# Kernel tuning notes

Hardware: AMD Instinct MI355X
Metric: run time of the kernel (lower is better)

Reference implementation:

```python
import jax, jax.numpy as jnp
import numpy as np

B, S, D = 2, 2048, 1024
H = 16
HD = D // H  # 64


def setup_inputs() -> dict:
    key = jax.random.key(0)
    ks = jax.random.split(key, 6)
    x = jax.random.normal(ks[0], (B, S, D), dtype=jnp.float32)
    sc = 1.0 / np.sqrt(D)
    Wq = jax.random.normal(ks[1], (D, D), dtype=jnp.float32) * sc
    Wk = jax.random.normal(ks[2], (D, D), dtype=jnp.float32) * sc
    Wv = jax.random.normal(ks[3], (D, D), dtype=jnp.float32) * sc
    Wo = jax.random.normal(ks[4], (D, D), dtype=jnp.float32) * sc
    bo = jax.random.normal(ks[5], (D,), dtype=jnp.float32) * 0.01
    return {"x": x, "Wq": Wq, "Wk": Wk, "Wv": Wv, "Wo": Wo, "bo": bo}


def reference(x, Wq, Wk, Wv, Wo, bo):
    b, s, d = x.shape
    # projections (torch Linear: y = x @ W.T; weights here stored as [d_in, d_out])
    Q = (x @ Wq).reshape(b, s, H, HD).transpose(0, 2, 1, 3)  # [b,h,s,hd]
    K = (x @ Wk).reshape(b, s, H, HD).transpose(0, 2, 1, 3)
    V = (x @ Wv).reshape(b, s, H, HD).transpose(0, 2, 1, 3)
    scores = jnp.einsum("bhqd,bhkd->bhqk", Q, K) / np.sqrt(HD)
    causal = jnp.triu(jnp.ones((s, s), dtype=bool), k=1)  # True above diagonal
    scores = jnp.where(causal[None, None], -jnp.inf, scores)
    attn = jax.nn.softmax(scores, axis=-1)
    # dropout_rate = 0.0 -> identity (eval-mode reference)
    ctx = jnp.einsum("bhqk,bhkd->bhqd", attn, V)
    ctx = ctx.transpose(0, 2, 1, 3).reshape(b, s, d)
    return ctx @ Wo + bo
```

## Files before the change

kernel.cpp:

```cpp
#include <hip/hip_runtime.h>
#include <hip/hip_bf16.h>

#define B_  2
#define S_  2048
#define D_  1024
#define H_  16
#define HD_ 64
#define M_  (B_*S_)

typedef __attribute__((ext_vector_type(8))) short short8;
typedef __attribute__((ext_vector_type(4))) float f32x4;

#define MFMA16(a, b, c) __builtin_amdgcn_mfma_f32_16x16x32_bf16((a), (b), (c), 0, 0, 0)

static __device__ inline short f2bf(float f) {
    union { float f; unsigned u; } v; v.f = f;
    unsigned r = v.u + 0x7FFFu + ((v.u >> 16) & 1u);
    return (short)(r >> 16);
}

static __device__ __forceinline__ float fexp2(float x) {
    float r;
    asm volatile("v_exp_f32 %0, %1\n\ts_nop 1" : "=v"(r) : "v"(x));
    return r;
}

static __device__ __forceinline__ unsigned cvt_pk_bf16(float lo, float hi) {
    unsigned r;
    asm volatile("v_cvt_pk_bf16_f32 %0, %1, %2" : "=v"(r) : "v"(lo), "v"(hi));
    return r;
}

static __device__ __forceinline__ void gl_lds16(const short* g, short* l) {
    __builtin_amdgcn_global_load_lds(
        (const __attribute__((address_space(1))) void*)g,
        (__attribute__((address_space(3))) void*)l, 16, 0, 0);
}

__global__ void prep_kernel(const float* __restrict__ x,
                            const float* __restrict__ Wq, const float* __restrict__ Wk,
                            const float* __restrict__ Wv, const float* __restrict__ Wo,
                            short* __restrict__ xb,
                            short* __restrict__ Wqkvt, short* __restrict__ Wot) {
    int z = blockIdx.z;
    if (z == 4) {
        int bid = blockIdx.y * 32 + blockIdx.x;
        int base = bid * 1024 + threadIdx.x;
#pragma unroll
        for (int it = 0; it < 4; ++it) {
            int i = base + it * 256;
            float4 v = ((const float4*)x)[i];
            short4 o;
            o.x = f2bf(v.x); o.y = f2bf(v.y); o.z = f2bf(v.z); o.w = f2bf(v.w);
            ((short4*)xb)[i] = o;
        }
        return;
    }
    __shared__ float tile[32][33];
    const float* W = (z == 0) ? Wq : (z == 1) ? Wk : (z == 2) ? Wv : Wo;
    short* Wt = (z == 3) ? Wot : (Wqkvt + ((size_t)z << 20));
    int tx = threadIdx.x & 31, ty = threadIdx.x >> 5;
    int n0 = blockIdx.x * 32, k0 = blockIdx.y * 32;
#pragma unroll
    for (int i = 0; i < 4; ++i)
        tile[ty + 8 * i][tx] = W[(size_t)(k0 + ty + 8 * i) * D_ + n0 + tx];
    __syncthreads();
#pragma unroll
    for (int i = 0; i < 4; ++i)
        Wt[(size_t)(n0 + ty + 8 * i) * D_ + k0 + tx] = f2bf(tile[tx][ty + 8 * i]);
}

__global__ __launch_bounds__(256) void gemm_qkv(const short* __restrict__ A,
                                                const short* __restrict__ Bt,
                                                short* __restrict__ out) {
    __shared__ __align__(16) short Asm[2][128 * 32];
    __shared__ __align__(16) short Bsm[2][128 * 32];
    const int NBX = 3;
    int X = blockIdx.x & 7, t = blockIdx.x >> 3;
    int bm = t / NBX, bn = X * NBX + t % NBX;
    int tid = threadIdx.x, l = tid & 63, w = tid >> 6;
    int lhi = l >> 4, llo = l & 15;
    int wm = w >> 1, wn = w & 1;

    f32x4 acc[4][4];
#pragma unroll
    for (int m = 0; m < 4; ++m)
#pragma unroll
        for (int n = 0; n < 4; ++n) acc[m][n] = (f32x4){0.f, 0.f, 0.f, 0.f};

    const short* Ag = A + (size_t)(bm * 128) * 1024;
    const short* Bg = Bt + (size_t)(bn * 128) * 1024;
    int c0 = tid, c1 = 256 + tid;
    int r0 = ((c0 >> 5) << 3) | (c0 & 7), s0 = ((c0 >> 3) & 3) ^ (r0 & 3);
    int r1 = ((c1 >> 5) << 3) | (c1 & 7), s1 = ((c1 >> 3) & 3) ^ (r1 & 3);

    auto stage = [&](int buf, int k0) {
        gl_lds16(Ag + (size_t)r0 * 1024 + k0 + s0 * 8, &Asm[buf][c0 * 8]);
        gl_lds16(Ag + (size_t)r1 * 1024 + k0 + s1 * 8, &Asm[buf][c1 * 8]);
        gl_lds16(Bg + (size_t)r0 * 1024 + k0 + s0 * 8, &Bsm[buf][c0 * 8]);
        gl_lds16(Bg + (size_t)r1 * 1024 + k0 + s1 * 8, &Bsm[buf][c1 * 8]);
    };

    int cia[4], cib[4];
#pragma unroll
    for (int m = 0; m < 4; ++m) {
        int row = wm * 64 + m * 16 + llo;
        cia[m] = ((row >> 3) << 5) | (((lhi ^ row) & 3) << 3) | (row & 7);
    }
#pragma unroll
    for (int n = 0; n < 4; ++n) {
        int row = wn * 64 + n * 16 + llo;
        cib[n] = ((row >> 3) << 5) | (((lhi ^ row) & 3) << 3) | (row & 7);
    }

    stage(0, 0);
    for (int i = 0; i < 32; ++i) {
        asm volatile("s_waitcnt vmcnt(0)" ::: "memory");
        __builtin_amdgcn_s_barrier();
        asm volatile("" ::: "memory");
        if (i + 1 < 32) stage((i + 1) & 1, (i + 1) * 32);
        int cur = i & 1;
        short8 af[4], bf[4];
#pragma unroll
        for (int m = 0; m < 4; ++m) af[m] = *(const short8*)&Asm[cur][cia[m] * 8];
#pragma unroll
        for (int n = 0; n < 4; ++n) bf[n] = *(const short8*)&Bsm[cur][cib[n] * 8];
#pragma unroll
        for (int m = 0; m < 4; ++m)
#pragma unroll
            for (int n = 0; n < 4; ++n)
                acc[m][n] = MFMA16(af[m], bf[n], acc[m][n]);
    }

    int rowb = bm * 128 + wm * 64, colb = bn * 128 + wn * 64;
#pragma unroll
    for (int m = 0; m < 4; ++m) {
#pragma unroll
        for (int n = 0; n < 4; ++n) {
            int col = colb + n * 16 + llo;
#pragma unroll
            for (int j = 0; j < 4; ++j) {
                int row = rowb + m * 16 + lhi * 4 + j;
                float v = acc[m][n][j];
                int proj = col >> 10, n1 = col & 1023;
                int h = n1 >> 6, hd = n1 & 63;
                int b = row >> 11, s = row & 2047;
                size_t off;
                if (proj == 0)
                    off = ((size_t)(b * 16 + h) * 2048 + s) * 64 + hd;
                else if (proj == 1)
                    off = (size_t)M_ * D_ + ((size_t)(b * 16 + h) * 2048 + s) * 64 + hd;
                else
                    off = (size_t)2 * M_ * D_ + ((size_t)(b * 16 + h) * 64 + hd) * 2048 + s;
                out[off] = f2bf(v);
            }
        }
    }
}

__global__ __launch_bounds__(256, 6) void gemm_out(const short* __restrict__ A,
                                                   const short* __restrict__ Bt,
                                                   const float* __restrict__ bias,
                                                   float* __restrict__ out) {
    __shared__ __align__(16) short Asm[2][64 * 32];
    __shared__ __align__(16) short Bsm[2][128 * 32];
    int bn = blockIdx.x & 7, bm = blockIdx.x >> 3;
    int tid = threadIdx.x, l = tid & 63, w = tid >> 6;
    int lhi = l >> 4, llo = l & 15;

    f32x4 acc[4][2];
#pragma unroll
    for (int m = 0; m < 4; ++m)
#pragma unroll
        for (int n = 0; n < 2; ++n) acc[m][n] = (f32x4){0.f, 0.f, 0.f, 0.f};

    const short* Ag = A + (size_t)(bm * 64) * 1024;
    const short* Bg = Bt + (size_t)(bn * 128) * 1024;
    int ca = tid;
    int ra = ((ca >> 5) << 3) | (ca & 7), sa = ((ca >> 3) & 3) ^ (ra & 3);
    int cb0 = tid, cb1 = tid + 256;
    int rb0 = ((cb0 >> 5) << 3) | (cb0 & 7), sb0 = ((cb0 >> 3) & 3) ^ (rb0 & 3);
    int rb1 = ((cb1 >> 5) << 3) | (cb1 & 7), sb1 = ((cb1 >> 3) & 3) ^ (rb1 & 3);

    auto stage = [&](int buf, int k0) {
        gl_lds16(Ag + (size_t)ra * 1024 + k0 + sa * 8, &Asm[buf][ca * 8]);
        gl_lds16(Bg + (size_t)rb0 * 1024 + k0 + sb0 * 8, &Bsm[buf][cb0 * 8]);
        gl_lds16(Bg + (size_t)rb1 * 1024 + k0 + sb1 * 8, &Bsm[buf][cb1 * 8]);
    };

    int cia[4], cib[2];
#pragma unroll
    for (int m = 0; m < 4; ++m) {
        int row = m * 16 + llo;
        cia[m] = ((row >> 3) << 5) | (((lhi ^ row) & 3) << 3) | (row & 7);
    }
#pragma unroll
    for (int n = 0; n < 2; ++n) {
        int row = w * 32 + n * 16 + llo;
        cib[n] = ((row >> 3) << 5) | (((lhi ^ row) & 3) << 3) | (row & 7);
    }

    stage(0, 0);
    for (int i = 0; i < 32; ++i) {
        asm volatile("s_waitcnt vmcnt(0)" ::: "memory");
        __builtin_amdgcn_s_barrier();
        asm volatile("" ::: "memory");
        if (i + 1 < 32) stage((i + 1) & 1, (i + 1) * 32);
        int cur = i & 1;
        short8 af[4], bf[2];
#pragma unroll
        for (int m = 0; m < 4; ++m) af[m] = *(const short8*)&Asm[cur][cia[m] * 8];
#pragma unroll
        for (int n = 0; n < 2; ++n) bf[n] = *(const short8*)&Bsm[cur][cib[n] * 8];
#pragma unroll
        for (int m = 0; m < 4; ++m)
#pragma unroll
            for (int n = 0; n < 2; ++n)
                acc[m][n] = MFMA16(af[m], bf[n], acc[m][n]);
    }

    int rowb = bm * 64, colb = bn * 128 + w * 32;
#pragma unroll
    for (int m = 0; m < 4; ++m)
#pragma unroll
        for (int n = 0; n < 2; ++n) {
            int col = colb + n * 16 + llo;
#pragma unroll
            for (int j = 0; j < 4; ++j) {
                int row = rowb + m * 16 + lhi * 4 + j;
                out[(size_t)row * 1024 + col] = acc[m][n][j] + bias[col];
            }
        }
}

__global__ __launch_bounds__(512) void attn_kernel(const short* __restrict__ Q,
                                                   const short* __restrict__ Kg,
                                                   const short* __restrict__ Vt,
                                                   short* __restrict__ ctx) {
    __shared__ __align__(16) char kvbuf[2][16384];
    __shared__ __align__(16) char plds[8][2048];
    int tid = threadIdx.x, w = tid >> 6, l = tid & 63;
    int lhi = l >> 4, llo = l & 15;
    int bh = blockIdx.x & 31, qp = blockIdx.x >> 5;
    int b = bh >> 4, h = bh & 15;
    char* pb = plds[w];

    const short* Qh = Q + (size_t)bh * S_ * HD_;
    const short* Kh = Kg + (size_t)bh * S_ * HD_;
    const short* Vh = Vt + (size_t)bh * HD_ * S_;

    int qbA = qp, qbB = 15 - qp;
    int NTA = 2 * qp + 2;
    const int NT = 34;

    int srow = tid >> 3;
    int ssrc = (16 * (tid & 7)) ^ ((srow & 7) << 4);
    auto stage = [&](char* buf, int c0) {
        gl_lds16(Kh + (size_t)(c0 + srow) * HD_ + (ssrc >> 1), (short*)(buf + tid * 16));
        gl_lds16(Vh + (size_t)srow * S_ + c0 + (ssrc >> 1), (short*)(buf + 8192 + tid * 16));
    };

    f32x4 O[4];
#pragma unroll
    for (int n = 0; n < 4; ++n) O[n] = (f32x4){0.f, 0.f, 0.f, 0.f};
    float lpart[4] = {0.f, 0.f, 0.f, 0.f};

    auto writeOut = [&](int qb) {
        int qbs = qb * 128 + w * 16;
#pragma unroll
        for (int j = 0; j < 4; ++j) {
            float ls = lpart[j];
            ls += __shfl_xor(ls, 1);
            ls += __shfl_xor(ls, 2);
            ls += __shfl_xor(ls, 4);
            ls += __shfl_xor(ls, 8);
            float inv = 1.0f / ls;
            int row = qbs + lhi * 4 + j;
            size_t base = ((size_t)(b * S_ + row)) * D_ + h * HD_;
#pragma unroll
            for (int n = 0; n < 4; ++n)
                ctx[base + n * 16 + llo] = f2bf(O[n][j] * inv);
        }
    };

    const float SC = 0.18033688f;
    const float M2 = 17.312340f;

    int qbase = qbA * 128 + w * 16;
    short8 aq0 = *(const short8*)(Qh + (size_t)(qbase + llo) * HD_ + 8 * lhi);
    short8 aq1 = *(const short8*)(Qh + (size_t)(qbase + llo) * HD_ + 32 + 8 * lhi);

    stage(kvbuf[0], 0);

    for (int i = 0; i < NT; ++i) {
        asm volatile("s_waitcnt vmcnt(0)" ::: "memory");
        __builtin_amdgcn_s_barrier();
        asm volatile("" ::: "memory");
        int kt = (i < NTA) ? i : i - NTA;
        int c0 = kt * 64;
        if (i + 1 < NT) {
            int ni = i + 1;
            int nkt = (ni < NTA) ? ni : ni - NTA;
            stage(kvbuf[ni & 1], nkt * 64);
        }
        const char* kb = kvbuf[i & 1];
        const char* vb = kb + 8192;

        if (c0 <= qbase + 15) {
            f32x4 sc4[4];
#pragma unroll
            for (int cb = 0; cb < 4; ++cb) {
                int row = cb * 16 + llo;
                int sw = (row & 7) << 4;
                short8 kf0 = *(const short8*)(kb + row * 128 + ((16 * lhi) ^ sw));
                short8 kf1 = *(const short8*)(kb + row * 128 + ((64 + 16 * lhi) ^ sw));
                f32x4 z = (f32x4){0.f, 0.f, 0.f, 0.f};
                z = MFMA16(aq0, kf0, z);
                z = MFMA16(aq1, kf1, z);
                sc4[cb] = z;
            }
            bool diag = (c0 + 63 > qbase);
#pragma unroll
            for (int j = 0; j < 4; ++j) {
                int qr = qbase + lhi * 4 + j;
                float v0 = fmaf(sc4[0][j], SC, -M2);
                float v1 = fmaf(sc4[1][j], SC, -M2);
                float v2 = fmaf(sc4[2][j], SC, -M2);
                float v3 = fmaf(sc4[3][j], SC, -M2);
                if (diag) {
                    if (c0 + llo > qr)      v0 = -1e30f;
                    if (c0 + 16 + llo > qr) v1 = -1e30f;
                    if (c0 + 32 + llo > qr) v2 = -1e30f;
                    if (c0 + 48 + llo > qr) v3 = -1e30f;
                }
                float p0 = fexp2(v0), p1 = fexp2(v1);
                float p2 = fexp2(v2), p3 = fexp2(v3);
                lpart[j] += (p0 + p1) + (p2 + p3);
                unsigned pk01 = cvt_pk_bf16(p0, p1);
                unsigned pk23 = cvt_pk_bf16(p2, p3);
                int r = lhi * 4 + j;
                char* rb = pb + r * 128;
                int sw = (r & 7) << 4;
                *(short*)(rb + ((2 * llo) ^ sw))      = (short)(pk01);
                *(short*)(rb + ((2 * llo + 32) ^ sw)) = (short)(pk01 >> 16);
                *(short*)(rb + ((2 * llo + 64) ^ sw)) = (short)(pk23);
                *(short*)(rb + ((2 * llo + 96) ^ sw)) = (short)(pk23 >> 16);
            }
            int swr = (llo & 7) << 4;
            short8 pa0 = *(const short8*)(pb + llo * 128 + ((16 * lhi) ^ swr));
            short8 pa1 = *(const short8*)(pb + llo * 128 + ((64 + 16 * lhi) ^ swr));
#pragma unroll
            for (int n = 0; n < 4; ++n) {
                int row = n * 16 + llo;
                int sw = (row & 7) << 4;
                short8 vf0 = *(const short8*)(vb + row * 128 + ((16 * lhi) ^ sw));
                short8 vf1 = *(const short8*)(vb + row * 128 + ((64 + 16 * lhi) ^ sw));
                O[n] = MFMA16(pa0, vf0, O[n]);
                O[n] = MFMA16(pa1, vf1, O[n]);
            }
        }

        if (i == NTA - 1) {
            writeOut(qbA);
#pragma unroll
            for (int n = 0; n < 4; ++n) O[n] = (f32x4){0.f, 0.f, 0.f, 0.f};
            lpart[0] = lpart[1] = lpart[2] = lpart[3] = 0.f;
            qbase = qbB * 128 + w * 16;
            aq0 = *(const short8*)(Qh + (size_t)(qbase + llo) * HD_ + 8 * lhi);
            aq1 = *(const short8*)(Qh + (size_t)(qbase + llo) * HD_ + 32 + 8 * lhi);
        }
    }
    writeOut(qbB);
}

extern "C" void kernel_launch(void* const* d_in, const int* in_sizes, int n_in,
                              void* d_out, int out_size, void* d_ws, size_t ws_size,
                              hipStream_t stream) {
    const float* x  = (const float*)d_in[0];
    const float* Wq = (const float*)d_in[1];
    const float* Wk = (const float*)d_in[2];
    const float* Wv = (const float*)d_in[3];
    const float* Wo = (const float*)d_in[4];
    const float* bo = (const float*)d_in[5];
    float* out = (float*)d_out;

    char* ws = (char*)d_ws;
    short* xb    = (short*)(ws);
    short* Wqkvt = (short*)(ws + (size_t)(8 << 20));
    short* Wot   = (short*)(ws + (size_t)(14 << 20));
    short* Qb    = (short*)(ws + (size_t)(16 << 20));
    short* Kb    = Qb + (size_t)M_ * D_;
    short* Vtb   = Qb + (size_t)2 * M_ * D_;
    short* ctx   = xb;

    prep_kernel<<<dim3(32, 32, 5), 256, 0, stream>>>(x, Wq, Wk, Wv, Wo, xb, Wqkvt, Wot);
    gemm_qkv<<<768, 256, 0, stream>>>(xb, Wqkvt, Qb);
    attn_kernel<<<256, 512, 0, stream>>>(Qb, Kb, Vtb, ctx);
    gemm_out<<<512, 256, 0, stream>>>(ctx, Wot, bo, out);
}
```

Measured before the change: 133.8 us.

## Give each attention wave two query sub-tiles and permute V layout for vector P stores

```diff
diff --git a/kernel.cpp b/kernel.cpp
--- a/kernel.cpp
+++ b/kernel.cpp
@@ -150,8 +150,10 @@
                     off = ((size_t)(b * 16 + h) * 2048 + s) * 64 + hd;
                 else if (proj == 1)
                     off = (size_t)M_ * D_ + ((size_t)(b * 16 + h) * 2048 + s) * 64 + hd;
-                else
-                    off = (size_t)2 * M_ * D_ + ((size_t)(b * 16 + h) * 64 + hd) * 2048 + s;
+                else {
+                    int sp = (s & ~63) | (4 * (s & 15) + ((s >> 4) & 3));
+                    off = (size_t)2 * M_ * D_ + ((size_t)(b * 16 + h) * 64 + hd) * 2048 + sp;
+                }
                 out[off] = f2bf(v);
             }
         }
@@ -233,12 +235,12 @@
         }
 }
 
-__global__ __launch_bounds__(512) void attn_kernel(const short* __restrict__ Q,
+__global__ __launch_bounds__(256) void attn_kernel(const short* __restrict__ Q,
                                                    const short* __restrict__ Kg,
                                                    const short* __restrict__ Vt,
                                                    short* __restrict__ ctx) {
     __shared__ __align__(16) char kvbuf[2][16384];
-    __shared__ __align__(16) char plds[8][2048];
+    __shared__ __align__(16) char plds[4][4096];
     int tid = threadIdx.x, w = tid >> 6, l = tid & 63;
     int lhi = l >> 4, llo = l & 15;
     int bh = blockIdx.x & 31, qp = blockIdx.x >> 5;
@@ -253,42 +255,55 @@
     int NTA = 2 * qp + 2;
     const int NT = 34;
 
-    int srow = tid >> 3;
-    int ssrc = (16 * (tid & 7)) ^ ((srow & 7) << 4);
+    int cc0 = tid, cc1 = tid + 256;
+    int r0 = cc0 >> 3, s0 = (16 * (cc0 & 7)) ^ ((r0 & 7) << 4);
+    int r1 = cc1 >> 3, s1 = (16 * (cc1 & 7)) ^ ((r1 & 7) << 4);
     auto stage = [&](char* buf, int c0) {
-        gl_lds16(Kh + (size_t)(c0 + srow) * HD_ + (ssrc >> 1), (short*)(buf + tid * 16));
-        gl_lds16(Vh + (size_t)srow * S_ + c0 + (ssrc >> 1), (short*)(buf + 8192 + tid * 16));
+        gl_lds16(Kh + (size_t)(c0 + r0) * HD_ + (s0 >> 1), (short*)(buf + cc0 * 16));
+        gl_lds16(Kh + (size_t)(c0 + r1) * HD_ + (s1 >> 1), (short*)(buf + cc1 * 16));
+        gl_lds16(Vh + (size_t)r0 * S_ + c0 + (s0 >> 1), (short*)(buf + 8192 + cc0 * 16));
+        gl_lds16(Vh + (size_t)r1 * S_ + c0 + (s1 >> 1), (short*)(buf + 8192 + cc1 * 16));
     };
 
-    f32x4 O[4];
-#pragma unroll
-    for (int n = 0; n < 4; ++n) O[n] = (f32x4){0.f, 0.f, 0.f, 0.f};
-    float lpart[4] = {0.f, 0.f, 0.f, 0.f};
-
-    auto writeOut = [&](int qb) {
-        int qbs = qb * 128 + w * 16;
-#pragma unroll
-        for (int j = 0; j < 4; ++j) {
-            float ls = lpart[j];
-            ls += __shfl_xor(ls, 1);
-            ls += __shfl_xor(ls, 2);
-            ls += __shfl_xor(ls, 4);
-            ls += __shfl_xor(ls, 8);
-            float inv = 1.0f / ls;
-            int row = qbs + lhi * 4 + j;
-            size_t base = ((size_t)(b * S_ + row)) * D_ + h * HD_;
-#pragma unroll
-            for (int n = 0; n < 4; ++n)
-                ctx[base + n * 16 + llo] = f2bf(O[n][j] * inv);
-        }
-    };
+    f32x4 O[2][4];
+    float lpart[2][4];
+#pragma unroll
+    for (int g = 0; g < 2; ++g)
+#pragma unroll
+        for (int n = 0; n < 4; ++n) {
+            O[g][n] = (f32x4){0.f, 0.f, 0.f, 0.f};
+            lpart[g][n] = 0.f;
+        }
 
     const float SC = 0.18033688f;
     const float M2 = 17.312340f;
 
-    int qbase = qbA * 128 + w * 16;
-    short8 aq0 = *(const short8*)(Qh + (size_t)(qbase + llo) * HD_ + 8 * lhi);
-    short8 aq1 = *(const short8*)(Qh + (size_t)(qbase + llo) * HD_ + 32 + 8 * lhi);
+    int qbw = qbA * 128 + w * 32;
+    short8 aq[2][2];
+#pragma unroll
+    for (int g = 0; g < 2; ++g) {
+        aq[g][0] = *(const short8*)(Qh + (size_t)(qbw + g * 16 + llo) * HD_ + 8 * lhi);
+        aq[g][1] = *(const short8*)(Qh + (size_t)(qbw + g * 16 + llo) * HD_ + 32 + 8 * lhi);
+    }
+
+    auto writeOut = [&](int qb) {
+#pragma unroll
+        for (int g = 0; g < 2; ++g)
+#pragma unroll
+            for (int j = 0; j < 4; ++j) {
+                float ls = lpart[g][j];
+                ls += __shfl_xor(ls, 1);
+                ls += __shfl_xor(ls, 2);
+                ls += __shfl_xor(ls, 4);
+                ls += __shfl_xor(ls, 8);
+                float inv = 1.0f / ls;
+                int row = qb * 128 + w * 32 + g * 16 + lhi * 4 + j;
+                size_t base = ((size_t)(b * S_ + row)) * D_ + h * HD_;
+#pragma unroll
+                for (int n = 0; n < 4; ++n)
+                    ctx[base + n * 16 + llo] = f2bf(O[g][n][j] * inv);
+            }
+    };
 
     stage(kvbuf[0], 0);
 
@@ -306,68 +321,91 @@
         const char* kb = kvbuf[i & 1];
         const char* vb = kb + 8192;
 
-        if (c0 <= qbase + 15) {
-            f32x4 sc4[4];
+        if (c0 <= qbw + 31) {
+            bool act0 = (c0 <= qbw + 15);
+            f32x4 sc4[2][4];
 #pragma unroll
             for (int cb = 0; cb < 4; ++cb) {
                 int row = cb * 16 + llo;
                 int sw = (row & 7) << 4;
                 short8 kf0 = *(const short8*)(kb + row * 128 + ((16 * lhi) ^ sw));
                 short8 kf1 = *(const short8*)(kb + row * 128 + ((64 + 16 * lhi) ^ sw));
-                f32x4 z = (f32x4){0.f, 0.f, 0.f, 0.f};
-                z = MFMA16(aq0, kf0, z);
-                z = MFMA16(aq1, kf1, z);
-                sc4[cb] = z;
-            }
-            bool diag = (c0 + 63 > qbase);
-#pragma unroll
-            for (int j = 0; j < 4; ++j) {
-                int qr = qbase + lhi * 4 + j;
-                float v0 = fmaf(sc4[0][j], SC, -M2);
-                float v1 = fmaf(sc4[1][j], SC, -M2);
-                float v2 = fmaf(sc4[2][j], SC, -M2);
-                float v3 = fmaf(sc4[3][j], SC, -M2);
-                if (diag) {
-                    if (c0 + llo > qr)      v0 = -1e30f;
-                    if (c0 + 16 + llo > qr) v1 = -1e30f;
-                    if (c0 + 32 + llo > qr) v2 = -1e30f;
-                    if (c0 + 48 + llo > qr) v3 = -1e30f;
+                f32x4 z1 = (f32x4){0.f, 0.f, 0.f, 0.f};
+                z1 = MFMA16(aq[1][0], kf0, z1);
+                z1 = MFMA16(aq[1][1], kf1, z1);
+                sc4[1][cb] = z1;
+                if (act0) {
+                    f32x4 z0 = (f32x4){0.f, 0.f, 0.f, 0.f};
+                    z0 = MFMA16(aq[0][0], kf0, z0);
+                    z0 = MFMA16(aq[0][1], kf1, z0);
+                    sc4[0][cb] = z0;
                 }
-                float p0 = fexp2(v0), p1 = fexp2(v1);
-                float p2 = fexp2(v2), p3 = fexp2(v3);
-                lpart[j] += (p0 + p1) + (p2 + p3);
-                unsigned pk01 = cvt_pk_bf16(p0, p1);
-                unsigned pk23 = cvt_pk_bf16(p2, p3);
-                int r = lhi * 4 + j;
-                char* rb = pb + r * 128;
-                int sw = (r & 7) << 4;
-                *(short*)(rb + ((2 * llo) ^ sw))      = (short)(pk01);
-                *(short*)(rb + ((2 * llo + 32) ^ sw)) = (short)(pk01 >> 16);
-                *(short*)(rb + ((2 * llo + 64) ^ sw)) = (short)(pk23);
-                *(short*)(rb + ((2 * llo + 96) ^ sw)) = (short)(pk23 >> 16);
-            }
-            int swr = (llo & 7) << 4;
-            short8 pa0 = *(const short8*)(pb + llo * 128 + ((16 * lhi) ^ swr));
-            short8 pa1 = *(const short8*)(pb + llo * 128 + ((64 + 16 * lhi) ^ swr));
+            }
+#pragma unroll
+            for (int g = 0; g < 2; ++g) {
+                if (g == 0 && !act0) continue;
+                bool diag = (c0 + 63 > qbw + g * 16);
+#pragma unroll
+                for (int j = 0; j < 4; ++j) {
+                    int qr = qbw + g * 16 + lhi * 4 + j;
+                    float v0 = fmaf(sc4[g][0][j], SC, -M2);
+                    float v1 = fmaf(sc4[g][1][j], SC, -M2);
+                    float v2 = fmaf(sc4[g][2][j], SC, -M2);
+                    float v3 = fmaf(sc4[g][3][j], SC, -M2);
+                    if (diag) {
+                        if (c0 + llo > qr)      v0 = -1e30f;
+                        if (c0 + 16 + llo > qr) v1 = -1e30f;
+                        if (c0 + 32 + llo > qr) v2 = -1e30f;
+                        if (c0 + 48 + llo > qr) v3 = -1e30f;
+                    }
+                    float p0 = fexp2(v0), p1 = fexp2(v1);
+                    float p2 = fexp2(v2), p3 = fexp2(v3);
+                    lpart[g][j] += (p0 + p1) + (p2 + p3);
+                    uint2 pk;
+                    pk.x = cvt_pk_bf16(p0, p1);
+                    pk.y = cvt_pk_bf16(p2, p3);
+                    int r = g * 16 + lhi * 4 + j;
+                    *(uint2*)(pb + r * 128 + ((8 * llo) ^ ((r & 7) << 4))) = pk;
+                }
+            }
+            short8 pa[2][2];
+#pragma unroll
+            for (int g = 0; g < 2; ++g) {
+                int rp = g * 16 + llo;
+                int swp = (rp & 7) << 4;
+                pa[g][0] = *(const short8*)(pb + rp * 128 + ((16 * lhi) ^ swp));
+                pa[g][1] = *(const short8*)(pb + rp * 128 + ((64 + 16 * lhi) ^ swp));
+            }
 #pragma unroll
             for (int n = 0; n < 4; ++n) {
                 int row = n * 16 + llo;
                 int sw = (row & 7) << 4;
                 short8 vf0 = *(const short8*)(vb + row * 128 + ((16 * lhi) ^ sw));
                 short8 vf1 = *(const short8*)(vb + row * 128 + ((64 + 16 * lhi) ^ sw));
-                O[n] = MFMA16(pa0, vf0, O[n]);
-                O[n] = MFMA16(pa1, vf1, O[n]);
+                O[1][n] = MFMA16(pa[1][0], vf0, O[1][n]);
+                O[1][n] = MFMA16(pa[1][1], vf1, O[1][n]);
+                if (act0) {
+                    O[0][n] = MFMA16(pa[0][0], vf0, O[0][n]);
+                    O[0][n] = MFMA16(pa[0][1], vf1, O[0][n]);
+                }
             }
         }
 
         if (i == NTA - 1) {
             writeOut(qbA);
 #pragma unroll
-            for (int n = 0; n < 4; ++n) O[n] = (f32x4){0.f, 0.f, 0.f, 0.f};
-            lpart[0] = lpart[1] = lpart[2] = lpart[3] = 0.f;
-            qbase = qbB * 128 + w * 16;
-            aq0 = *(const short8*)(Qh + (size_t)(qbase + llo) * HD_ + 8 * lhi);
-            aq1 = *(const short8*)(Qh + (size_t)(qbase + llo) * HD_ + 32 + 8 * lhi);
+            for (int g = 0; g < 2; ++g)
+#pragma unroll
+                for (int n = 0; n < 4; ++n) {
+                    O[g][n] = (f32x4){0.f, 0.f, 0.f, 0.f};
+                    lpart[g][n] = 0.f;
+                }
+            qbw = qbB * 128 + w * 32;
+#pragma unroll
+            for (int g = 0; g < 2; ++g) {
+                aq[g][0] = *(const short8*)(Qh + (size_t)(qbw + g * 16 + llo) * HD_ + 8 * lhi);
+                aq[g][1] = *(const short8*)(Qh + (size_t)(qbw + g * 16 + llo) * HD_ + 32 + 8 * lhi);
+            }
         }
     }
     writeOut(qbB);
@@ -395,6 +433,6 @@
 
     prep_kernel<<<dim3(32, 32, 5), 256, 0, stream>>>(x, Wq, Wk, Wv, Wo, xb, Wqkvt, Wot);
     gemm_qkv<<<768, 256, 0, stream>>>(xb, Wqkvt, Qb);
-    attn_kernel<<<256, 512, 0, stream>>>(Qb, Kb, Vtb, ctx);
+    attn_kernel<<<256, 256, 0, stream>>>(Qb, Kb, Vtb, ctx);
     gemm_out<<<512, 256, 0, stream>>>(ctx, Wot, bo, out);
 }
```

Result: slower. 175.7 us (+31.3%).

## Split attention into 64-row query blocks with 4 waves, vectorize P LDS writes

Applied to the files above, without the earlier changes.

```diff
diff --git a/kernel.cpp b/kernel.cpp
--- a/kernel.cpp
+++ b/kernel.cpp
@@ -150,8 +150,10 @@
                     off = ((size_t)(b * 16 + h) * 2048 + s) * 64 + hd;
                 else if (proj == 1)
                     off = (size_t)M_ * D_ + ((size_t)(b * 16 + h) * 2048 + s) * 64 + hd;
-                else
-                    off = (size_t)2 * M_ * D_ + ((size_t)(b * 16 + h) * 64 + hd) * 2048 + s;
+                else {
+                    int sp = (s & ~63) | (4 * (s & 15) + ((s >> 4) & 3));
+                    off = (size_t)2 * M_ * D_ + ((size_t)(b * 16 + h) * 64 + hd) * 2048 + sp;
+                }
                 out[off] = f2bf(v);
             }
         }
@@ -233,15 +235,15 @@
         }
 }
 
-__global__ __launch_bounds__(512) void attn_kernel(const short* __restrict__ Q,
-                                                   const short* __restrict__ Kg,
-                                                   const short* __restrict__ Vt,
-                                                   short* __restrict__ ctx) {
+__global__ __launch_bounds__(256, 4) void attn_kernel(const short* __restrict__ Q,
+                                                      const short* __restrict__ Kg,
+                                                      const short* __restrict__ Vt,
+                                                      short* __restrict__ ctx) {
     __shared__ __align__(16) char kvbuf[2][16384];
-    __shared__ __align__(16) char plds[8][2048];
+    __shared__ __align__(16) char plds[4][2048];
     int tid = threadIdx.x, w = tid >> 6, l = tid & 63;
     int lhi = l >> 4, llo = l & 15;
-    int bh = blockIdx.x & 31, qp = blockIdx.x >> 5;
+    int bh = blockIdx.x & 31, p = blockIdx.x >> 5;
     int b = bh >> 4, h = bh & 15;
     char* pb = plds[w];
 
@@ -249,15 +251,18 @@
     const short* Kh = Kg + (size_t)bh * S_ * HD_;
     const short* Vh = Vt + (size_t)bh * HD_ * S_;
 
-    int qbA = qp, qbB = 15 - qp;
-    int NTA = 2 * qp + 2;
-    const int NT = 34;
-
-    int srow = tid >> 3;
-    int ssrc = (16 * (tid & 7)) ^ ((srow & 7) << 4);
+    int qsA = p, qsB = 31 - p;
+    int NTA = p + 1;
+    const int NT = 33;
+
+    int cc0 = tid, cc1 = tid + 256;
+    int r0 = cc0 >> 3, s0 = (16 * (cc0 & 7)) ^ ((r0 & 7) << 4);
+    int r1 = cc1 >> 3, s1 = (16 * (cc1 & 7)) ^ ((r1 & 7) << 4);
     auto stage = [&](char* buf, int c0) {
-        gl_lds16(Kh + (size_t)(c0 + srow) * HD_ + (ssrc >> 1), (short*)(buf + tid * 16));
-        gl_lds16(Vh + (size_t)srow * S_ + c0 + (ssrc >> 1), (short*)(buf + 8192 + tid * 16));
+        gl_lds16(Kh + (size_t)(c0 + r0) * HD_ + (s0 >> 1), (short*)(buf + cc0 * 16));
+        gl_lds16(Kh + (size_t)(c0 + r1) * HD_ + (s1 >> 1), (short*)(buf + cc1 * 16));
+        gl_lds16(Vh + (size_t)r0 * S_ + c0 + (s0 >> 1), (short*)(buf + 8192 + cc0 * 16));
+        gl_lds16(Vh + (size_t)r1 * S_ + c0 + (s1 >> 1), (short*)(buf + 8192 + cc1 * 16));
     };
 
     f32x4 O[4];
@@ -265,8 +270,7 @@
     for (int n = 0; n < 4; ++n) O[n] = (f32x4){0.f, 0.f, 0.f, 0.f};
     float lpart[4] = {0.f, 0.f, 0.f, 0.f};
 
-    auto writeOut = [&](int qb) {
-        int qbs = qb * 128 + w * 16;
+    auto writeOut = [&](int qbase) {
 #pragma unroll
         for (int j = 0; j < 4; ++j) {
             float ls = lpart[j];
@@ -275,7 +279,7 @@
             ls += __shfl_xor(ls, 4);
             ls += __shfl_xor(ls, 8);
             float inv = 1.0f / ls;
-            int row = qbs + lhi * 4 + j;
+            int row = qbase + lhi * 4 + j;
             size_t base = ((size_t)(b * S_ + row)) * D_ + h * HD_;
 #pragma unroll
             for (int n = 0; n < 4; ++n)
@@ -286,7 +290,7 @@
     const float SC = 0.18033688f;
     const float M2 = 17.312340f;
 
-    int qbase = qbA * 128 + w * 16;
+    int qbase = qsA * 64 + w * 16;
     short8 aq0 = *(const short8*)(Qh + (size_t)(qbase + llo) * HD_ + 8 * lhi);
     short8 aq1 = *(const short8*)(Qh + (size_t)(qbase + llo) * HD_ + 32 + 8 * lhi);
 
@@ -336,15 +340,11 @@
                 float p0 = fexp2(v0), p1 = fexp2(v1);
                 float p2 = fexp2(v2), p3 = fexp2(v3);
                 lpart[j] += (p0 + p1) + (p2 + p3);
-                unsigned pk01 = cvt_pk_bf16(p0, p1);
-                unsigned pk23 = cvt_pk_bf16(p2, p3);
+                uint2 pk;
+                pk.x = cvt_pk_bf16(p0, p1);
+                pk.y = cvt_pk_bf16(p2, p3);
                 int r = lhi * 4 + j;
-                char* rb = pb + r * 128;
-                int sw = (r & 7) << 4;
-                *(short*)(rb + ((2 * llo) ^ sw))      = (short)(pk01);
-                *(short*)(rb + ((2 * llo + 32) ^ sw)) = (short)(pk01 >> 16);
-                *(short*)(rb + ((2 * llo + 64) ^ sw)) = (short)(pk23);
-                *(short*)(rb + ((2 * llo + 96) ^ sw)) = (short)(pk23 >> 16);
+                *(uint2*)(pb + r * 128 + ((8 * llo) ^ ((r & 7) << 4))) = pk;
             }
             int swr = (llo & 7) << 4;
             short8 pa0 = *(const short8*)(pb + llo * 128 + ((16 * lhi) ^ swr));
@@ -361,16 +361,16 @@
         }
 
         if (i == NTA - 1) {
-            writeOut(qbA);
+            writeOut(qsA * 64 + w * 16);
 #pragma unroll
             for (int n = 0; n < 4; ++n) O[n] = (f32x4){0.f, 0.f, 0.f, 0.f};
             lpart[0] = lpart[1] = lpart[2] = lpart[3] = 0.f;
-            qbase = qbB * 128 + w * 16;
+            qbase = qsB * 64 + w * 16;
             aq0 = *(const short8*)(Qh + (size_t)(qbase + llo) * HD_ + 8 * lhi);
             aq1 = *(const short8*)(Qh + (size_t)(qbase + llo) * HD_ + 32 + 8 * lhi);
         }
     }
-    writeOut(qbB);
+    writeOut(qsB * 64 + w * 16);
 }
 
 extern "C" void kernel_launch(void* const* d_in, const int* in_sizes, int n_in,
@@ -395,6 +395,6 @@
 
     prep_kernel<<<dim3(32, 32, 5), 256, 0, stream>>>(x, Wq, Wk, Wv, Wo, xb, Wqkvt, Wot);
     gemm_qkv<<<768, 256, 0, stream>>>(xb, Wqkvt, Qb);
-    attn_kernel<<<256, 512, 0, stream>>>(Qb, Kb, Vtb, ctx);
+    attn_kernel<<<512, 256, 0, stream>>>(Qb, Kb, Vtb, ctx);
     gemm_out<<<512, 256, 0, stream>>>(ctx, Wot, bo, out);
 }
```

After: 137.1 us. 1.02x slower.

## Load GEMM A operand directly from global into registers, staging only B in LDS

Applied to the files above, without the earlier changes.

```diff
diff --git a/kernel.cpp b/kernel.cpp
--- a/kernel.cpp
+++ b/kernel.cpp
@@ -73,11 +73,10 @@
 __global__ __launch_bounds__(256) void gemm_qkv(const short* __restrict__ A,
                                                 const short* __restrict__ Bt,
                                                 short* __restrict__ out) {
-    __shared__ __align__(16) short Asm[2][128 * 32];
     __shared__ __align__(16) short Bsm[2][128 * 32];
     const int NBX = 3;
-    int X = blockIdx.x & 7, t = blockIdx.x >> 3;
-    int bm = t / NBX, bn = X * NBX + t % NBX;
+    int X = blockIdx.x & 7, t0 = blockIdx.x >> 3;
+    int bm = t0 / NBX, bn = X * NBX + t0 % NBX;
     int tid = threadIdx.x, l = tid & 63, w = tid >> 6;
     int lhi = l >> 4, llo = l & 15;
     int wm = w >> 1, wn = w & 1;
@@ -90,46 +89,54 @@
 
     const short* Ag = A + (size_t)(bm * 128) * 1024;
     const short* Bg = Bt + (size_t)(bn * 128) * 1024;
+    const short* Ap = Ag + (size_t)(wm * 64 + llo) * 1024 + 8 * lhi;
     int c0 = tid, c1 = 256 + tid;
     int r0 = ((c0 >> 5) << 3) | (c0 & 7), s0 = ((c0 >> 3) & 3) ^ (r0 & 3);
     int r1 = ((c1 >> 5) << 3) | (c1 & 7), s1 = ((c1 >> 3) & 3) ^ (r1 & 3);
 
-    auto stage = [&](int buf, int k0) {
-        gl_lds16(Ag + (size_t)r0 * 1024 + k0 + s0 * 8, &Asm[buf][c0 * 8]);
-        gl_lds16(Ag + (size_t)r1 * 1024 + k0 + s1 * 8, &Asm[buf][c1 * 8]);
+    auto stageB = [&](int buf, int k0) {
         gl_lds16(Bg + (size_t)r0 * 1024 + k0 + s0 * 8, &Bsm[buf][c0 * 8]);
         gl_lds16(Bg + (size_t)r1 * 1024 + k0 + s1 * 8, &Bsm[buf][c1 * 8]);
     };
-
-    int cia[4], cib[4];
-#pragma unroll
-    for (int m = 0; m < 4; ++m) {
-        int row = wm * 64 + m * 16 + llo;
-        cia[m] = ((row >> 3) << 5) | (((lhi ^ row) & 3) << 3) | (row & 7);
-    }
+    auto loadA = [&](short8* dst, int k0) {
+#pragma unroll
+        for (int m = 0; m < 4; ++m)
+            dst[m] = *(const short8*)(Ap + (size_t)m * 16 * 1024 + k0);
+    };
+
+    int cib[4];
 #pragma unroll
     for (int n = 0; n < 4; ++n) {
         int row = wn * 64 + n * 16 + llo;
         cib[n] = ((row >> 3) << 5) | (((lhi ^ row) & 3) << 3) | (row & 7);
     }
 
-    stage(0, 0);
-    for (int i = 0; i < 32; ++i) {
+    auto compute = [&](const short8* af, const short* bs) {
+        short8 bf[4];
+#pragma unroll
+        for (int n = 0; n < 4; ++n) bf[n] = *(const short8*)&bs[cib[n] * 8];
+#pragma unroll
+        for (int m = 0; m < 4; ++m)
+#pragma unroll
+            for (int n = 0; n < 4; ++n)
+                acc[m][n] = MFMA16(af[m], bf[n], acc[m][n]);
+    };
+
+    short8 afA[4], afB[4];
+    stageB(0, 0);
+    loadA(afA, 0);
+#pragma unroll 1
+    for (int t = 0; t < 16; ++t) {
         asm volatile("s_waitcnt vmcnt(0)" ::: "memory");
         __builtin_amdgcn_s_barrier();
         asm volatile("" ::: "memory");
-        if (i + 1 < 32) stage((i + 1) & 1, (i + 1) * 32);
-        int cur = i & 1;
-        short8 af[4], bf[4];
-#pragma unroll
-        for (int m = 0; m < 4; ++m) af[m] = *(const short8*)&Asm[cur][cia[m] * 8];
-#pragma unroll
-        for (int n = 0; n < 4; ++n) bf[n] = *(const short8*)&Bsm[cur][cib[n] * 8];
-#pragma unroll
-        for (int m = 0; m < 4; ++m)
-#pragma unroll
-            for (int n = 0; n < 4; ++n)
-                acc[m][n] = MFMA16(af[m], bf[n], acc[m][n]);
+        if (2 * t + 1 < 32) { stageB(1, (2 * t + 1) * 32); loadA(afB, (2 * t + 1) * 32); }
+        compute(afA, Bsm[0]);
+        asm volatile("s_waitcnt vmcnt(0)" ::: "memory");
+        __builtin_amdgcn_s_barrier();
+        asm volatile("" ::: "memory");
+        if (2 * t + 2 < 32) { stageB(0, (2 * t + 2) * 32); loadA(afA, (2 * t + 2) * 32); }
+        compute(afB, Bsm[1]);
     }
 
     int rowb = bm * 128 + wm * 64, colb = bn * 128 + wn * 64;
@@ -158,11 +165,10 @@
     }
 }
 
-__global__ __launch_bounds__(256, 6) void gemm_out(const short* __restrict__ A,
+__global__ __launch_bounds__(256, 4) void gemm_out(const short* __restrict__ A,
                                                    const short* __restrict__ Bt,
                                                    const float* __restrict__ bias,
                                                    float* __restrict__ out) {
-    __shared__ __align__(16) short Asm[2][64 * 32];
     __shared__ __align__(16) short Bsm[2][128 * 32];
     int bn = blockIdx.x & 7, bm = blockIdx.x >> 3;
     int tid = threadIdx.x, l = tid & 63, w = tid >> 6;
@@ -176,47 +182,54 @@
 
     const short* Ag = A + (size_t)(bm * 64) * 1024;
     const short* Bg = Bt + (size_t)(bn * 128) * 1024;
-    int ca = tid;
-    int ra = ((ca >> 5) << 3) | (ca & 7), sa = ((ca >> 3) & 3) ^ (ra & 3);
-    int cb0 = tid, cb1 = tid + 256;
-    int rb0 = ((cb0 >> 5) << 3) | (cb0 & 7), sb0 = ((cb0 >> 3) & 3) ^ (rb0 & 3);
-    int rb1 = ((cb1 >> 5) << 3) | (cb1 & 7), sb1 = ((cb1 >> 3) & 3) ^ (rb1 & 3);
-
-    auto stage = [&](int buf, int k0) {
-        gl_lds16(Ag + (size_t)ra * 1024 + k0 + sa * 8, &Asm[buf][ca * 8]);
-        gl_lds16(Bg + (size_t)rb0 * 1024 + k0 + sb0 * 8, &Bsm[buf][cb0 * 8]);
-        gl_lds16(Bg + (size_t)rb1 * 1024 + k0 + sb1 * 8, &Bsm[buf][cb1 * 8]);
-    };
-
-    int cia[4], cib[2];
-#pragma unroll
-    for (int m = 0; m < 4; ++m) {
-        int row = m * 16 + llo;
-        cia[m] = ((row >> 3) << 5) | (((lhi ^ row) & 3) << 3) | (row & 7);
-    }
+    const short* Ap = Ag + (size_t)llo * 1024 + 8 * lhi;
+    int c0 = tid, c1 = 256 + tid;
+    int r0 = ((c0 >> 5) << 3) | (c0 & 7), s0 = ((c0 >> 3) & 3) ^ (r0 & 3);
+    int r1 = ((c1 >> 5) << 3) | (c1 & 7), s1 = ((c1 >> 3) & 3) ^ (r1 & 3);
+
+    auto stageB = [&](int buf, int k0) {
+        gl_lds16(Bg + (size_t)r0 * 1024 + k0 + s0 * 8, &Bsm[buf][c0 * 8]);
+        gl_lds16(Bg + (size_t)r1 * 1024 + k0 + s1 * 8, &Bsm[buf][c1 * 8]);
+    };
+    auto loadA = [&](short8* dst, int k0) {
+#pragma unroll
+        for (int m = 0; m < 4; ++m)
+            dst[m] = *(const short8*)(Ap + (size_t)m * 16 * 1024 + k0);
+    };
+
+    int cib[2];
 #pragma unroll
     for (int n = 0; n < 2; ++n) {
         int row = w * 32 + n * 16 + llo;
         cib[n] = ((row >> 3) << 5) | (((lhi ^ row) & 3) << 3) | (row & 7);
     }
 
-    stage(0, 0);
-    for (int i = 0; i < 32; ++i) {
+    auto compute = [&](const short8* af, const short* bs) {
+        short8 bf[2];
+#pragma unroll
+        for (int n = 0; n < 2; ++n) bf[n] = *(const short8*)&bs[cib[n] * 8];
+#pragma unroll
+        for (int m = 0; m < 4; ++m)
+#pragma unroll
+            for (int n = 0; n < 2; ++n)
+                acc[m][n] = MFMA16(af[m], bf[n], acc[m][n]);
+    };
+
+    short8 afA[4], afB[4];
+    stageB(0, 0);
+    loadA(afA, 0);
+#pragma unroll 1
+    for (int t = 0; t < 16; ++t) {
         asm volatile("s_waitcnt vmcnt(0)" ::: "memory");
         __builtin_amdgcn_s_barrier();
         asm volatile("" ::: "memory");
-        if (i + 1 < 32) stage((i + 1) & 1, (i + 1) * 32);
-        int cur = i & 1;
-        short8 af[4], bf[2];
-#pragma unroll
-        for (int m = 0; m < 4; ++m) af[m] = *(const short8*)&Asm[cur][cia[m] * 8];
-#pragma unroll
-        for (int n = 0; n < 2; ++n) bf[n] = *(const short8*)&Bsm[cur][cib[n] * 8];
-#pragma unroll
-        for (int m = 0; m < 4; ++m)
-#pragma unroll
-            for (int n = 0; n < 2; ++n)
-                acc[m][n] = MFMA16(af[m], bf[n], acc[m][n]);
+        if (2 * t + 1 < 32) { stageB(1, (2 * t + 1) * 32); loadA(afB, (2 * t + 1) * 32); }
+        compute(afA, Bsm[0]);
+        asm volatile("s_waitcnt vmcnt(0)" ::: "memory");
+        __builtin_amdgcn_s_barrier();
+        asm volatile("" ::: "memory");
+        if (2 * t + 2 < 32) { stageB(0, (2 * t + 2) * 32); loadA(afA, (2 * t + 2) * 32); }
+        compute(afB, Bsm[1]);
     }
 
     int rowb = bm * 64, colb = bn * 128 + w * 32;
```

Result: slower. 181.1 us (+35.4%).
